# Kernel optimization log

Measured on AMD Instinct MI355X. Metric: run time of the kernel, lower is better.

## Reference

```python
import jax, jax.numpy as jnp
import numpy as np

B = 16
N = [4096, 1024, 256, 64, 16]
NF = [1, 16, 32, 64, 128, 256]
DEG = 6
KS = 5
LAT = 32


def spline_conv(x, edge_index, pseudo, W, root, bias):
    """SplineConv: open B-spline, degree 1, dim 3, kernel_size 5, sum aggregation (norm=False).
    x: [Nn, Cin], edge_index: [2, E] (src, dst), pseudo: [E, 3] in [0,1], W: [125, Cin, Cout]."""
    src, dst = edge_index[0], edge_index[1]
    v = pseudo * (KS - 1)                       # degree-1 open spline interval
    lo = jnp.clip(jnp.floor(v), 0.0, KS - 2)
    frac = v - lo                               # [E, 3]
    lo = lo.astype(jnp.int32)
    xs = x[src]                                 # [E, Cin] gather
    strides = jnp.array([1, KS, KS * KS], dtype=jnp.int32)
    msg = jnp.zeros((src.shape[0], W.shape[2]), dtype=x.dtype)
    for s in range(8):                          # (degree+1)^dim = 8 basis products
        bits = np.array([(s >> d) & 1 for d in range(3)], dtype=np.int32)
        basis = jnp.prod(jnp.where(bits[None, :] == 1, frac, 1.0 - frac), axis=1)  # [E]
        kidx = jnp.sum((lo + bits[None, :]) * strides[None, :], axis=1)            # [E]
        Wg = W[kidx]                                                               # [E, Cin, Cout]
        msg = msg + basis[:, None] * jnp.einsum('ei,eio->eo', xs, Wg)
    agg = jax.ops.segment_sum(msg, dst, num_segments=x.shape[0])
    return agg + x @ root + bias


def _fwd(fl, ei):
    (x, ea0, ea1, ea2, ea3, ea4, P01, P12, P23, P34, Pn1, P1n, P43, P32, P21, P10,
     W_c1, r_c1, b_c1, W_c2, r_c2, b_c2, W_c3, r_c3, b_c3, W_c4, r_c4, b_c4, W_c5, r_c5, b_c5,
     W_d5, r_d5, b_d5, W_d4, r_d4, b_d4, W_d3, r_d3, b_d3, W_d2, r_d2, b_d2, W_d1, r_d1, b_d1,
     fce1_w, fce1_b, fce21_w, fce21_b, fce22_w, fce22_b, fcd3_w, fcd3_b, fcd4_w, fcd4_b, eps) = fl
    ei0, ei1, ei2, ei3, ei4 = ei
    elu = jax.nn.elu
    # ---- encoder ----
    h = elu(spline_conv(x, ei0, ea0, W_c1, r_c1, b_c1))
    h = P01 @ h.reshape(B, N[0], NF[1])
    h = elu(spline_conv(h.reshape(-1, NF[1]), ei1, ea1, W_c2, r_c2, b_c2))
    h = P12 @ h.reshape(B, N[1], NF[2])
    h = elu(spline_conv(h.reshape(-1, NF[2]), ei2, ea2, W_c3, r_c3, b_c3))
    h = P23 @ h.reshape(B, N[2], NF[3])
    h = elu(spline_conv(h.reshape(-1, NF[3]), ei3, ea3, W_c4, r_c4, b_c4))
    h = P34 @ h.reshape(B, N[3], NF[4])
    h = elu(spline_conv(h.reshape(-1, NF[4]), ei4, ea4, W_c5, r_c5, b_c5))
    h = (Pn1 @ h.reshape(B, N[4], NF[5])).reshape(B, NF[5])
    # 1x1 convs over [B, C, 1, 1] == dense layers
    h = elu(h @ fce1_w + fce1_b)
    mu = h @ fce21_w + fce21_b
    logvar = h @ fce22_w + fce22_b
    # ---- reparameterize ----
    z = eps * jnp.exp(0.5 * logvar) + mu
    # ---- decoder ----
    h = elu(z @ fcd3_w + fcd3_b)
    h = elu(h @ fcd4_w + fcd4_b)
    h = P1n @ h.reshape(B, 1, NF[5])            # [B, N4, nf5]
    h = elu(spline_conv(h.reshape(-1, NF[5]), ei4, ea4, W_d5, r_d5, b_d5))
    h = P43 @ h.reshape(B, N[4], NF[4])
    h = elu(spline_conv(h.reshape(-1, NF[4]), ei3, ea3, W_d4, r_d4, b_d4))
    h = P32 @ h.reshape(B, N[3], NF[3])
    h = elu(spline_conv(h.reshape(-1, NF[3]), ei2, ea2, W_d3, r_d3, b_d3))
    h = P21 @ h.reshape(B, N[2], NF[2])
    h = elu(spline_conv(h.reshape(-1, NF[2]), ei1, ea1, W_d2, r_d2, b_d2))
    h = P10 @ h.reshape(B, N[1], NF[1])
    h = elu(spline_conv(h.reshape(-1, NF[1]), ei0, ea0, W_d1, r_d1, b_d1))
    recon = h.reshape(B, -1)                    # [B, N0] (nf0 == 1)
    return recon, mu, logvar


def setup_inputs() -> dict:
    key = jax.random.key(0)
    ks = iter(jax.random.split(key, 128))
    def nrm(shape, scale=1.0):
        return jax.random.normal(next(ks), shape, dtype=jnp.float32) * scale
    def edges(n):
        # per-sample random mesh-like connectivity, offset per graph copy
        e = jax.random.randint(next(ks), (2, B, n * DEG), 0, n)
        off = (jnp.arange(B) * n)[None, :, None]
        return (e + off).reshape(2, -1).astype(jnp.int32)
    inp = {}
    inp['x'] = nrm((B * N[0], NF[0]))
    for i in range(5):
        inp[f'ea{i}'] = jax.random.uniform(next(ks), (B * N[i] * DEG, 3), dtype=jnp.float32)
    pools = {'P01': (N[1], N[0]), 'P12': (N[2], N[1]), 'P23': (N[3], N[2]), 'P34': (N[4], N[3]),
             'Pn1': (1, N[4]), 'P1n': (N[4], 1), 'P43': (N[3], N[4]), 'P32': (N[2], N[3]),
             'P21': (N[1], N[2]), 'P10': (N[0], N[1])}
    for k2, (a, b) in pools.items():
        inp[k2] = nrm((a, b), 1.0 / np.sqrt(b))
    def spl(name, ci, co):
        inp[f'W_{name}'] = nrm((KS ** 3, ci, co), 0.1 / np.sqrt(ci))
        inp[f'r_{name}'] = nrm((ci, co), 1.0 / np.sqrt(ci))
        inp[f'b_{name}'] = nrm((co,), 0.01)
    spl('c1', NF[0], NF[1]); spl('c2', NF[1], NF[2]); spl('c3', NF[2], NF[3]); spl('c4', NF[3], NF[4]); spl('c5', NF[4], NF[5])
    spl('d5', NF[5], NF[4]); spl('d4', NF[4], NF[3]); spl('d3', NF[3], NF[2]); spl('d2', NF[2], NF[1]); spl('d1', NF[1], NF[0])
    def lin(name, ci, co):
        inp[f'{name}_w'] = nrm((ci, co), 1.0 / np.sqrt(ci))
        inp[f'{name}_b'] = nrm((co,), 0.01)
    lin('fce1', NF[5], NF[5]); lin('fce21', NF[5], LAT); lin('fce22', NF[5], LAT)
    lin('fcd3', LAT, NF[5]); lin('fcd4', NF[5], NF[5])
    inp['eps'] = nrm((B, LAT))
    for i in range(5):
        inp[f'ei{i}'] = edges(N[i])
    return inp


def reference(x, ea0, ea1, ea2, ea3, ea4, P01, P12, P23, P34, Pn1, P1n, P43, P32, P21, P10,
              W_c1, r_c1, b_c1, W_c2, r_c2, b_c2, W_c3, r_c3, b_c3, W_c4, r_c4, b_c4, W_c5, r_c5, b_c5,
              W_d5, r_d5, b_d5, W_d4, r_d4, b_d4, W_d3, r_d3, b_d3, W_d2, r_d2, b_d2, W_d1, r_d1, b_d1,
              fce1_w, fce1_b, fce21_w, fce21_b, fce22_w, fce22_b, fcd3_w, fcd3_b, fcd4_w, fcd4_b, eps,
              ei0, ei1, ei2, ei3, ei4):
    fl = (x, ea0, ea1, ea2, ea3, ea4, P01, P12, P23, P34, Pn1, P1n, P43, P32, P21, P10,
          W_c1, r_c1, b_c1, W_c2, r_c2, b_c2, W_c3, r_c3, b_c3, W_c4, r_c4, b_c4, W_c5, r_c5, b_c5,
          W_d5, r_d5, b_d5, W_d4, r_d4, b_d4, W_d3, r_d3, b_d3, W_d2, r_d2, b_d2, W_d1, r_d1, b_d1,
          fce1_w, fce1_b, fce21_w, fce21_b, fce22_w, fce22_b, fcd3_w, fcd3_b, fcd4_w, fcd4_b, eps)
    return _fwd(fl, (ei0, ei1, ei2, ei3, ei4))
```

## Files before the change

### kernel.cpp

```cpp
#include <hip/hip_runtime.h>
#include <hip/hip_bf16.h>

#define TPB 256
#define CDIV(a,b) (((a)+(b)-1)/(b))

__device__ __forceinline__ float elu_f(float v) {
    return v > 0.f ? v : expm1f(v);
}

__device__ __forceinline__ int ld_idx(const void* __restrict__ ei, int pos, int is64) {
    if (is64) return (int)((const long long*)ei)[pos];
    return ((const int*)ei)[pos];
}

__device__ __forceinline__ void spline_basis(const float* __restrict__ pseudo, int e,
                                             float bas[8], int kidx[8]) {
    float f[3]; int lo[3];
#pragma unroll
    for (int d = 0; d < 3; ++d) {
        float v = pseudo[e * 3 + d] * 4.f;
        float l = floorf(v);
        l = fminf(fmaxf(l, 0.f), 3.f);
        f[d] = v - l;
        lo[d] = (int)l;
    }
#pragma unroll
    for (int s = 0; s < 8; ++s) {
        int b0 = s & 1, b1 = (s >> 1) & 1, b2 = (s >> 2) & 1;
        bas[s] = (b0 ? f[0] : 1.f - f[0]) * (b1 ? f[1] : 1.f - f[1]) * (b2 ? f[2] : 1.f - f[2]);
        kidx[s] = (lo[0] + b0) + 5 * (lo[1] + b1) + 25 * (lo[2] + b2);
    }
}

__global__ void k_detect(const int* __restrict__ ei0_as_i32, int* __restrict__ flag) {
    if (threadIdx.x == 0 && blockIdx.x == 0) {
        int zeros = 0;
        for (int k = 0; k < 128; ++k)
            if (ei0_as_i32[2 * k + 1] == 0) zeros++;
        flag[0] = (zeros >= 120) ? 1 : 0;
    }
}

__global__ __launch_bounds__(TPB) void k_zero(float* __restrict__ p, int n) {
    int t = blockIdx.x * blockDim.x + threadIdx.x;
    if (t < n) p[t] = 0.f;
}

__global__ __launch_bounds__(TPB) void k_zero_i(int* __restrict__ p, int n) {
    int t = blockIdx.x * blockDim.x + threadIdx.x;
    if (t < n) p[t] = 0;
}

__global__ __launch_bounds__(TPB) void k_csr_count5(const void* e0, const void* e1,
                                                    const void* e2, const void* e3,
                                                    const void* e4, int* __restrict__ cnt,
                                                    const int* __restrict__ flag) {
    int t = blockIdx.x * blockDim.x + threadIdx.x;
    if (t >= 523776) return;
    int is64 = flag[0];
    const void* ei; int e, E, noff;
    if (t < 393216)      { ei = e0; e = t;          E = 393216; noff = 0; }
    else if (t < 491520) { ei = e1; e = t - 393216; E = 98304;  noff = 65536; }
    else if (t < 516096) { ei = e2; e = t - 491520; E = 24576;  noff = 81920; }
    else if (t < 522240) { ei = e3; e = t - 516096; E = 6144;   noff = 86016; }
    else                 { ei = e4; e = t - 522240; E = 1536;   noff = 87040; }
    int dst = ld_idx(ei, E + e, is64);
    atomicAdd(&cnt[noff + dst], 1);
}

__device__ __forceinline__ void lvl_of_block(int b, int& l, int& lb) {
    if (b < 256)      { l = 0; lb = b; }
    else if (b < 320) { l = 1; lb = b - 256; }
    else if (b < 336) { l = 2; lb = b - 320; }
    else if (b < 340) { l = 3; lb = b - 336; }
    else              { l = 4; lb = b - 340; }
}

__global__ __launch_bounds__(256) void k_scan_a(const int* __restrict__ cnt,
                                                int* __restrict__ rows,
                                                int* __restrict__ bsum) {
    const int NOFF[5] = {0, 65536, 81920, 86016, 87040};
    const int ROFF[5] = {0, 65537, 81922, 86019, 87044};
    __shared__ int s[256];
    int l, lb; lvl_of_block(blockIdx.x, l, lb);
    int t = threadIdx.x;
    int i = lb * 256 + t;
    int v = cnt[NOFF[l] + i];
    s[t] = v;
    __syncthreads();
    for (int off = 1; off < 256; off <<= 1) {
        int u = (t >= off) ? s[t - off] : 0;
        __syncthreads();
        s[t] += u;
        __syncthreads();
    }
    rows[ROFF[l] + i] = s[t] - v;
    if (t == 255) bsum[blockIdx.x] = s[255];
}

__global__ __launch_bounds__(256) void k_scan_b(int* __restrict__ bsum,
                                                int* __restrict__ rows) {
    const int NB[5]    = {256, 64, 16, 4, 1};
    const int BOFF[5]  = {0, 256, 320, 336, 340};
    const int ROFF[5]  = {0, 65537, 81922, 86019, 87044};
    const int NODES[5] = {65536, 16384, 4096, 1024, 256};
    __shared__ int s[256];
    int l = blockIdx.x, t = threadIdx.x;
    int nb = NB[l];
    int v = (t < nb) ? bsum[BOFF[l] + t] : 0;
    s[t] = v;
    __syncthreads();
    for (int off = 1; off < 256; off <<= 1) {
        int u = (t >= off) ? s[t - off] : 0;
        __syncthreads();
        s[t] += u;
        __syncthreads();
    }
    if (t < nb) bsum[BOFF[l] + t] = s[t] - v;
    if (t == 0) rows[ROFF[l] + NODES[l]] = s[255];
}

__global__ __launch_bounds__(256) void k_scan_c(const int* __restrict__ bsum,
                                                int* __restrict__ rows) {
    const int ROFF[5] = {0, 65537, 81922, 86019, 87044};
    int l, lb; lvl_of_block(blockIdx.x, l, lb);
    rows[ROFF[l] + lb * 256 + threadIdx.x] += bsum[blockIdx.x];
}

__global__ __launch_bounds__(TPB) void k_csr_fill5(const void* e0, const void* e1,
                                                   const void* e2, const void* e3,
                                                   const void* e4,
                                                   const int* __restrict__ rows,
                                                   int* __restrict__ cur,
                                                   int* __restrict__ eids,
                                                   const int* __restrict__ flag) {
    int t = blockIdx.x * blockDim.x + threadIdx.x;
    if (t >= 523776) return;
    int is64 = flag[0];
    const void* ei; int e, E, noff, roff, eoff;
    if (t < 393216)      { ei = e0; e = t;          E = 393216; noff = 0;     roff = 0;     eoff = 0; }
    else if (t < 491520) { ei = e1; e = t - 393216; E = 98304;  noff = 65536; roff = 65537; eoff = 393216; }
    else if (t < 516096) { ei = e2; e = t - 491520; E = 24576;  noff = 81920; roff = 81922; eoff = 491520; }
    else if (t < 522240) { ei = e3; e = t - 516096; E = 6144;   noff = 86016; roff = 86019; eoff = 516096; }
    else                 { ei = e4; e = t - 522240; E = 1536;   noff = 87040; roff = 87044; eoff = 522240; }
    int dst = ld_idx(ei, E + e, is64);
    int pos = rows[roff + dst] + atomicAdd(&cur[noff + dst], 1);
    eids[eoff + pos] = e;
}

__global__ __launch_bounds__(TPB) void k_csr_count(const void* __restrict__ ei,
                                                   int* __restrict__ cnt, int E,
                                                   const int* __restrict__ flag) {
    int t = blockIdx.x * blockDim.x + threadIdx.x;
    if (t >= E) return;
    int dst = ld_idx(ei, E + t, flag[0]);
    atomicAdd(&cnt[dst], 1);
}

__global__ __launch_bounds__(1024) void k_csr_scan(const int* __restrict__ cnt,
                                                   int* __restrict__ row_ptr) {
    __shared__ int s_part[1024];
    int t = threadIdx.x;
    int base = t * 64;
    int sum = 0;
    for (int i = 0; i < 64; ++i) sum += cnt[base + i];
    s_part[t] = sum;
    __syncthreads();
    for (int off = 1; off < 1024; off <<= 1) {
        int v = (t >= off) ? s_part[t - off] : 0;
        __syncthreads();
        s_part[t] += v;
        __syncthreads();
    }
    int run = (t == 0) ? 0 : s_part[t - 1];
    for (int i = 0; i < 64; ++i) { row_ptr[base + i] = run; run += cnt[base + i]; }
    if (t == 1023) row_ptr[65536] = run;
}

__global__ __launch_bounds__(TPB) void k_csr_fill(const void* __restrict__ ei,
                                                  const int* __restrict__ row_ptr,
                                                  int* __restrict__ cur,
                                                  int* __restrict__ eid, int E,
                                                  const int* __restrict__ flag) {
    int t = blockIdx.x * blockDim.x + threadIdx.x;
    if (t >= E) return;
    int dst = ld_idx(ei, E + t, flag[0]);
    int pos = row_ptr[dst] + atomicAdd(&cur[dst], 1);
    eid[pos] = t;
}

__global__ __launch_bounds__(256) void k_gather_c1(const float* __restrict__ x,
                                                   const float* __restrict__ pseudo,
                                                   const void* __restrict__ ei,
                                                   const float* __restrict__ W,
                                                   const float* __restrict__ root,
                                                   const float* __restrict__ bias,
                                                   const int* __restrict__ row_ptr,
                                                   const int* __restrict__ eid,
                                                   float* __restrict__ agg,
                                                   const int* __restrict__ flag) {
    __shared__ float4 s_w[500];
    for (int i = threadIdx.x; i < 500; i += 256)
        s_w[i] = reinterpret_cast<const float4*>(W)[i];
    __syncthreads();
    int t = blockIdx.x * 256 + threadIdx.x;
    int n = t >> 2, cg = t & 3, co0 = cg * 4;
    int is64 = flag[0];
    float xn = x[n];
    float a0 = fmaf(xn, root[co0 + 0], bias[co0 + 0]);
    float a1 = fmaf(xn, root[co0 + 1], bias[co0 + 1]);
    float a2 = fmaf(xn, root[co0 + 2], bias[co0 + 2]);
    float a3 = fmaf(xn, root[co0 + 3], bias[co0 + 3]);
    int rb = row_ptr[n], re = row_ptr[n + 1];
    for (int idx = rb; idx < re; ++idx) {
        int e = eid[idx];
        int src = ld_idx(ei, e, is64);
        float bas[8]; int kidx[8];
        spline_basis(pseudo, e, bas, kidx);
        float xs = x[src];
        float m0 = 0.f, m1 = 0.f, m2 = 0.f, m3 = 0.f;
#pragma unroll
        for (int s = 0; s < 8; ++s) {
            float4 w = s_w[kidx[s] * 4 + cg];
            float bs = bas[s];
            m0 = fmaf(bs, w.x, m0);
            m1 = fmaf(bs, w.y, m1);
            m2 = fmaf(bs, w.z, m2);
            m3 = fmaf(bs, w.w, m3);
        }
        a0 = fmaf(xs, m0, a0);
        a1 = fmaf(xs, m1, a1);
        a2 = fmaf(xs, m2, a2);
        a3 = fmaf(xs, m3, a3);
    }
    float4 v = make_float4(a0, a1, a2, a3);
    *reinterpret_cast<float4*>(&agg[n * 16 + co0]) = v;
}

__global__ __launch_bounds__(256) void k_gather_d1(const float* __restrict__ xin,
                                                   const float* __restrict__ pseudo,
                                                   const void* __restrict__ ei,
                                                   const float* __restrict__ W,
                                                   const float* __restrict__ root,
                                                   const float* __restrict__ bias,
                                                   const int* __restrict__ row_ptr,
                                                   const int* __restrict__ eid,
                                                   float* __restrict__ outp,
                                                   const int* __restrict__ flag) {
    __shared__ float s_w[2000];
    for (int i = threadIdx.x; i < 2000; i += 256) s_w[i] = W[i];
    __syncthreads();
    int t = blockIdx.x * 256 + threadIdx.x;
    int n = t >> 2, l = t & 3;
    int is64 = flag[0];
    int rb = row_ptr[n], re = row_ptr[n + 1];
    float acc = 0.f;
    for (int idx = rb + l; idx < re; idx += 4) {
        int e = eid[idx];
        int src = ld_idx(ei, e, is64);
        float bas[8]; int kidx[8];
        spline_basis(pseudo, e, bas, kidx);
        const float4* xs4 = reinterpret_cast<const float4*>(xin + src * 16);
        float4 xv0 = xs4[0], xv1 = xs4[1], xv2 = xs4[2], xv3 = xs4[3];
        float m = 0.f;
#pragma unroll
        for (int s = 0; s < 8; ++s) {
            const float4* wp = reinterpret_cast<const float4*>(s_w + kidx[s] * 16);
            float4 w0 = wp[0], w1 = wp[1], w2 = wp[2], w3 = wp[3];
            float p = 0.f;
            p = fmaf(xv0.x, w0.x, p); p = fmaf(xv0.y, w0.y, p);
            p = fmaf(xv0.z, w0.z, p); p = fmaf(xv0.w, w0.w, p);
            p = fmaf(xv1.x, w1.x, p); p = fmaf(xv1.y, w1.y, p);
            p = fmaf(xv1.z, w1.z, p); p = fmaf(xv1.w, w1.w, p);
            p = fmaf(xv2.x, w2.x, p); p = fmaf(xv2.y, w2.y, p);
            p = fmaf(xv2.z, w2.z, p); p = fmaf(xv2.w, w2.w, p);
            p = fmaf(xv3.x, w3.x, p); p = fmaf(xv3.y, w3.y, p);
            p = fmaf(xv3.z, w3.z, p); p = fmaf(xv3.w, w3.w, p);
            m = fmaf(bas[s], p, m);
        }
        acc += m;
    }
    acc += __shfl_xor(acc, 1);
    acc += __shfl_xor(acc, 2);
    if (l == 0) {
        const float4* xr = reinterpret_cast<const float4*>(xin + n * 16);
        const float4* rr = reinterpret_cast<const float4*>(root);
        float r = bias[0];
#pragma unroll
        for (int q = 0; q < 4; ++q) {
            float4 xv = xr[q], rv = rr[q];
            r = fmaf(xv.x, rv.x, r); r = fmaf(xv.y, rv.y, r);
            r = fmaf(xv.z, rv.z, r); r = fmaf(xv.w, rv.w, r);
        }
        outp[n] = elu_f(r + acc);
    }
}

template <int CIN, int COUT, int CSPLIT, int IROOT>
__global__ __launch_bounds__(256) void k_gW2(const float* __restrict__ x,
                                             const float* __restrict__ pseudo,
                                             const void* __restrict__ ei,
                                             const float* __restrict__ W,
                                             const float* __restrict__ root,
                                             const float* __restrict__ bias,
                                             const int* __restrict__ row_ptr,
                                             const int* __restrict__ eid,
                                             float* __restrict__ agg,
                                             const int* __restrict__ flag) {
    constexpr int COG = COUT / 4;
    constexpr int CPT = CIN / CSPLIT;
    constexpr int PS = CPT + 1;
    __shared__ float4 s_w[125 * PS];
    int cg = blockIdx.y, cih = blockIdx.z;
    const float4* W4 = reinterpret_cast<const float4*>(W);
    for (int i = threadIdx.x; i < 125 * CPT; i += 256) {
        int k = i / CPT, ci = i - k * CPT;
        s_w[k * PS + ci] = W4[(k * CIN + cih * CPT + ci) * COG + cg];
    }
    __syncthreads();
    int nl = threadIdx.x >> 2, l = threadIdx.x & 3;
    int n = blockIdx.x * 64 + nl;
    int is64 = flag[0];
    int co0 = cg * 4;
    float4 acc = make_float4(0.f, 0.f, 0.f, 0.f);
    if (IROOT == 1 || (IROOT == 2 && cih == 0)) {
        if (l == 0) acc = reinterpret_cast<const float4*>(bias)[cg];
        constexpr int CQ = CIN / 4;
        const float* xp = x + (size_t)n * CIN + l * CQ;
        const float4* r4 = reinterpret_cast<const float4*>(root) + (size_t)(l * CQ) * COG + cg;
#pragma unroll 4
        for (int ci = 0; ci < CQ; ++ci) {
            float xv = xp[ci];
            float4 rv = r4[ci * COG];
            acc.x = fmaf(xv, rv.x, acc.x); acc.y = fmaf(xv, rv.y, acc.y);
            acc.z = fmaf(xv, rv.z, acc.z); acc.w = fmaf(xv, rv.w, acc.w);
        }
    }
    int rb = row_ptr[n], re = row_ptr[n + 1];
    for (int idx = rb + l; idx < re; idx += 4) {
        int e = eid[idx];
        int src = ld_idx(ei, e, is64);
        float bas[8]; int kidx[8];
        spline_basis(pseudo, e, bas, kidx);
        float xv[CPT];
        const float* xp = x + (size_t)src * CIN + cih * CPT;
#pragma unroll
        for (int ci = 0; ci < CPT; ++ci) xv[ci] = xp[ci];
#pragma unroll
        for (int s = 0; s < 8; ++s) {
            const float4* wp = s_w + kidx[s] * PS;
            float bs = bas[s];
#pragma unroll
            for (int ci = 0; ci < CPT; ++ci) {
                float bx = bs * xv[ci];
                float4 w = wp[ci];
                acc.x = fmaf(bx, w.x, acc.x); acc.y = fmaf(bx, w.y, acc.y);
                acc.z = fmaf(bx, w.z, acc.z); acc.w = fmaf(bx, w.w, acc.w);
            }
        }
    }
    acc.x += __shfl_xor(acc.x, 1); acc.y += __shfl_xor(acc.y, 1);
    acc.z += __shfl_xor(acc.z, 1); acc.w += __shfl_xor(acc.w, 1);
    acc.x += __shfl_xor(acc.x, 2); acc.y += __shfl_xor(acc.y, 2);
    acc.z += __shfl_xor(acc.z, 2); acc.w += __shfl_xor(acc.w, 2);
    if (l == 0) {
        float* o = agg + (size_t)n * COUT + co0;
        if (IROOT == 1) {
            *reinterpret_cast<float4*>(o) = acc;
        } else {
            atomicAdd(o + 0, acc.x); atomicAdd(o + 1, acc.y);
            atomicAdd(o + 2, acc.z); atomicAdd(o + 3, acc.w);
        }
    }
}

__global__ __launch_bounds__(TPB) void k_root4(const float* __restrict__ x,
                                               const float* __restrict__ root,
                                               const float* __restrict__ bias,
                                               float* __restrict__ out,
                                               int nnode, int cin, int cout) {
    int t = blockIdx.x * blockDim.x + threadIdx.x;
    if (t >= nnode * cout) return;
    int n = t / cout, co = t - n * cout;
    const float4* xr = reinterpret_cast<const float4*>(x + n * cin);
    float a0 = 0.f, a1 = 0.f, a2 = 0.f, a3 = 0.f;
    int q4 = cin >> 2;
    for (int q = 0; q < q4; ++q) {
        float4 xv = xr[q];
        const float* rp = root + (q * 4) * cout + co;
        a0 = fmaf(xv.x, rp[0], a0);
        a1 = fmaf(xv.y, rp[cout], a1);
        a2 = fmaf(xv.z, rp[2 * cout], a2);
        a3 = fmaf(xv.w, rp[3 * cout], a3);
    }
    out[t] = bias[co] + ((a0 + a1) + (a2 + a3));
}

template <int CIN, int COUT, int CSPLIT>
__global__ __launch_bounds__(TPB) void k_msg4(const float* __restrict__ x,
                                              const float* __restrict__ pseudo,
                                              const void* __restrict__ ei,
                                              const float* __restrict__ W,
                                              float* __restrict__ agg, int E,
                                              const int* __restrict__ flag) {
    constexpr int COG = COUT / 4;
    constexpr int CPT = CIN / CSPLIT;
    int t = blockIdx.x * blockDim.x + threadIdx.x;
    if (t >= E * COG * CSPLIT) return;
    int is64 = flag[0];
    int cog = t % COG;
    int rest = t / COG;
    int cs = rest % CSPLIT;
    int e = rest / CSPLIT;
    int co0 = cog * 4;
    int src = ld_idx(ei, e, is64);
    int dst = ld_idx(ei, E + e, is64);
    float bas[8]; int kidx[8];
    spline_basis(pseudo, e, bas, kidx);
    int wof[8];
#pragma unroll
    for (int s = 0; s < 8; ++s) wof[s] = kidx[s] * CIN * COUT + co0;
    float a0 = 0.f, a1 = 0.f, a2 = 0.f, a3 = 0.f;
    const float* xp = x + src * CIN + cs * CPT;
    const int cbase = cs * CPT * COUT;
    for (int ci = 0; ci < CPT; ++ci) {
        float xv = xp[ci];
        int off = cbase + ci * COUT;
#pragma unroll
        for (int s = 0; s < 8; ++s) {
            float4 w = *reinterpret_cast<const float4*>(&W[wof[s] + off]);
            float bx = bas[s] * xv;
            a0 = fmaf(bx, w.x, a0);
            a1 = fmaf(bx, w.y, a1);
            a2 = fmaf(bx, w.z, a2);
            a3 = fmaf(bx, w.w, a3);
        }
    }
    float* ap = &agg[dst * COUT + co0];
    atomicAdd(ap + 0, a0);
    atomicAdd(ap + 1, a1);
    atomicAdd(ap + 2, a2);
    atomicAdd(ap + 3, a3);
}

template <int CIN, int COUT>
__global__ __launch_bounds__(TPB) void k_msg_s(const float* __restrict__ x,
                                               const float* __restrict__ pseudo,
                                               const void* __restrict__ ei,
                                               const float* __restrict__ W,
                                               float* __restrict__ agg, int E,
                                               const int* __restrict__ flag) {
    int t = blockIdx.x * blockDim.x + threadIdx.x;
    if (t >= E * COUT) return;
    int is64 = flag[0];
    int e = t / COUT, co = t - e * COUT;
    int src = ld_idx(ei, e, is64);
    int dst = ld_idx(ei, E + e, is64);
    float bas[8]; int kidx[8];
    spline_basis(pseudo, e, bas, kidx);
    float acc = 0.f;
    const float* xp = x + src * CIN;
    for (int ci = 0; ci < CIN; ++ci) {
        float xv = xp[ci];
#pragma unroll
        for (int s = 0; s < 8; ++s)
            acc = fmaf(bas[s] * xv, W[kidx[s] * CIN * COUT + ci * COUT + co], acc);
    }
    atomicAdd(&agg[dst * COUT + co], acc);
}

__global__ __launch_bounds__(1024) void k_msg_c1(const float* __restrict__ x,
                                                 const float* __restrict__ pseudo,
                                                 const void* __restrict__ ei,
                                                 const float* __restrict__ W,
                                                 const float* __restrict__ root,
                                                 const float* __restrict__ bias,
                                                 float* __restrict__ agg,
                                                 const int* __restrict__ flag) {
    __shared__ float s_acc[4096 * 4];
    __shared__ float s_w[125 * 4];
    int b = blockIdx.x, cg = blockIdx.y, t = threadIdx.x;
    int co0 = cg * 4;
    int is64 = flag[0];
    if (t < 500) s_w[t] = W[(t >> 2) * 16 + co0 + (t & 3)];
    float r0 = root[co0], r1 = root[co0 + 1], r2 = root[co0 + 2], r3 = root[co0 + 3];
    float b0 = bias[co0], b1 = bias[co0 + 1], b2 = bias[co0 + 2], b3 = bias[co0 + 3];
    for (int n = t; n < 4096; n += 1024) {
        float xv = x[b * 4096 + n];
        s_acc[n * 4 + 0] = fmaf(xv, r0, b0);
        s_acc[n * 4 + 1] = fmaf(xv, r1, b1);
        s_acc[n * 4 + 2] = fmaf(xv, r2, b2);
        s_acc[n * 4 + 3] = fmaf(xv, r3, b3);
    }
    __syncthreads();
    int ebeg = b * 24576;
    for (int k = t; k < 24576; k += 1024) {
        int e = ebeg + k;
        int src = ld_idx(ei, e, is64);
        int dst = ld_idx(ei, 393216 + e, is64);
        float xv = x[src];
        float bas[8]; int kidx[8];
        spline_basis(pseudo, e, bas, kidx);
        float m0 = 0.f, m1 = 0.f, m2 = 0.f, m3 = 0.f;
#pragma unroll
        for (int s = 0; s < 8; ++s) {
            const float* wp = s_w + kidx[s] * 4;
            float bs = bas[s];
            m0 = fmaf(bs, wp[0], m0);
            m1 = fmaf(bs, wp[1], m1);
            m2 = fmaf(bs, wp[2], m2);
            m3 = fmaf(bs, wp[3], m3);
        }
        int dl = (dst - b * 4096) * 4;
        atomicAdd(&s_acc[dl + 0], m0 * xv);
        atomicAdd(&s_acc[dl + 1], m1 * xv);
        atomicAdd(&s_acc[dl + 2], m2 * xv);
        atomicAdd(&s_acc[dl + 3], m3 * xv);
    }
    __syncthreads();
    for (int n = t; n < 4096; n += 1024) {
        float4 v = *reinterpret_cast<float4*>(&s_acc[n * 4]);
        *reinterpret_cast<float4*>(&agg[(b * 4096 + n) * 16 + co0]) = v;
    }
}

template <int F, int ELU>
__global__ __launch_bounds__(256) void k_pool2(const float* __restrict__ in,
                                               const float* __restrict__ P,
                                               float* __restrict__ out,
                                               int nout, int nin) {
    constexpr int FQ = F / 4;
    constexpr int TI = 256 / FQ;
    constexpr int KT = 64;
    constexpr int PS = KT + 4;
    __shared__ float s_p[TI * PS];
    __shared__ float4 s_in[KT * FQ];
    int tid = threadIdx.x;
    int fq = tid % FQ;
    int i = tid / FQ;
    int b = blockIdx.y;
    int gi = blockIdx.x * TI + i;
    int nchunk = nin / gridDim.z;
    int kbeg = blockIdx.z * nchunk;
    const float4* inb4 = reinterpret_cast<const float4*>(in + b * nin * F);
    float4 acc = make_float4(0.f, 0.f, 0.f, 0.f);

    for (int k0 = kbeg; k0 < kbeg + nchunk; k0 += KT) {
        __syncthreads();
        for (int idx = tid; idx < TI * (KT / 4); idx += 256) {
            int r = idx / (KT / 4), c = idx % (KT / 4);
            float4 v = *reinterpret_cast<const float4*>(&P[(blockIdx.x * TI + r) * nin + k0 + c * 4]);
            *reinterpret_cast<float4*>(&s_p[r * PS + c * 4]) = v;
        }
        for (int idx = tid; idx < KT * FQ; idx += 256) {
            float4 v = inb4[(size_t)(k0 + idx / FQ) * FQ + (idx % FQ)];
            if (ELU) {
                v.x = elu_f(v.x); v.y = elu_f(v.y);
                v.z = elu_f(v.z); v.w = elu_f(v.w);
            }
            s_in[idx] = v;
        }
        __syncthreads();
#pragma unroll 4
        for (int j = 0; j < KT; j += 4) {
            float4 pv = *reinterpret_cast<const float4*>(&s_p[i * PS + j]);
            float4 v0 = s_in[(j + 0) * FQ + fq];
            float4 v1 = s_in[(j + 1) * FQ + fq];
            float4 v2 = s_in[(j + 2) * FQ + fq];
            float4 v3 = s_in[(j + 3) * FQ + fq];
            acc.x = fmaf(pv.x, v0.x, acc.x); acc.y = fmaf(pv.x, v0.y, acc.y);
            acc.z = fmaf(pv.x, v0.z, acc.z); acc.w = fmaf(pv.x, v0.w, acc.w);
            acc.x = fmaf(pv.y, v1.x, acc.x); acc.y = fmaf(pv.y, v1.y, acc.y);
            acc.z = fmaf(pv.y, v1.z, acc.z); acc.w = fmaf(pv.y, v1.w, acc.w);
            acc.x = fmaf(pv.z, v2.x, acc.x); acc.y = fmaf(pv.z, v2.y, acc.y);
            acc.z = fmaf(pv.z, v2.z, acc.z); acc.w = fmaf(pv.z, v2.w, acc.w);
            acc.x = fmaf(pv.w, v3.x, acc.x); acc.y = fmaf(pv.w, v3.y, acc.y);
            acc.z = fmaf(pv.w, v3.z, acc.z); acc.w = fmaf(pv.w, v3.w, acc.w);
        }
    }
    float* o = out + ((size_t)b * nout + gi) * F + fq * 4;
    if (gridDim.z > 1) {
        atomicAdd(o + 0, acc.x); atomicAdd(o + 1, acc.y);
        atomicAdd(o + 2, acc.z); atomicAdd(o + 3, acc.w);
    } else {
        *reinterpret_cast<float4*>(o) = acc;
    }
}

__global__ __launch_bounds__(TPB) void k_pool_e(const float* __restrict__ in,
                                                const float* __restrict__ P,
                                                float* __restrict__ out,
                                                int nout, int nin, int F, int elu) {
    int t = blockIdx.x * blockDim.x + threadIdx.x;
    if (t >= 16 * nout * F) return;
    int f = t % F;
    int rest = t / F;
    int i = rest % nout;
    int b = rest / nout;
    const float* ip = in + b * nin * F + f;
    const float* pp = P + i * nin;
    float acc = 0.f;
    if (elu) {
#pragma unroll 4
        for (int j = 0; j < nin; ++j) acc = fmaf(pp[j], elu_f(ip[j * F]), acc);
    } else {
#pragma unroll 4
        for (int j = 0; j < nin; ++j) acc = fmaf(pp[j], ip[j * F], acc);
    }
    out[t] = acc;
}

__global__ __launch_bounds__(1024) void k_fc_fused2(
        const float* __restrict__ c5agg, const float* __restrict__ Pn1,
        const float* __restrict__ fce1_w, const float* __restrict__ fce1_b,
        const float* __restrict__ fce21_w, const float* __restrict__ fce21_b,
        const float* __restrict__ fce22_w, const float* __restrict__ fce22_b,
        const float* __restrict__ eps,
        const float* __restrict__ fcd3_w, const float* __restrict__ fcd3_b,
        const float* __restrict__ fcd4_w, const float* __restrict__ fcd4_b,
        const float* __restrict__ P1n,
        float* __restrict__ out_mu, float* __restrict__ out_lv,
        float* __restrict__ dec_in) {
    __shared__ float s0[256], s1[256], sz[32], sp[1024];
    int b = blockIdx.x, t = threadIdx.x;
    if (t < 256) {
        const float* ap = c5agg + b * 4096 + t;
        float acc = 0.f;
#pragma unroll
        for (int n = 0; n < 16; ++n) acc = fmaf(Pn1[n], elu_f(ap[n * 256]), acc);
        s0[t] = acc;
    }
    __syncthreads();
    {
        int q = t >> 8, co = t & 255;
        const float* w = fce1_w + co;
        float a = 0.f;
        int c0 = q * 64;
        for (int ci = 0; ci < 64; ci += 8) {
#pragma unroll
            for (int k = 0; k < 8; ++k) a = fmaf(s0[c0 + ci + k], w[(c0 + ci + k) * 256], a);
        }
        sp[t] = a;
    }
    __syncthreads();
    if (t < 256) s1[t] = elu_f(sp[t] + sp[t + 256] + sp[t + 512] + sp[t + 768] + fce1_b[t]);
    __syncthreads();
    if (t < 512) {
        int which = t >> 8, r = t & 255;
        int co = r & 31, q = r >> 5;
        const float* w = (which ? fce22_w : fce21_w) + co;
        float a = 0.f;
        int c0 = q * 32;
#pragma unroll
        for (int k = 0; k < 32; ++k) a = fmaf(s1[c0 + k], w[(c0 + k) * 32], a);
        sp[t] = a;
    }
    __syncthreads();
    if (t < 64) {
        int which = t >> 5, co = t & 31;
        float m = (which ? fce22_b : fce21_b)[co];
        int base = which * 256 + co;
#pragma unroll
        for (int q = 0; q < 8; ++q) m += sp[base + q * 32];
        if (which == 0) { out_mu[b * 32 + co] = m; s0[co] = m; }
        else            { out_lv[b * 32 + co] = m; s0[64 + co] = m; }
    }
    __syncthreads();
    if (t < 32) sz[t] = fmaf(eps[b * 32 + t], expf(0.5f * s0[64 + t]), s0[t]);
    __syncthreads();
    if (t < 256) {
        float d = fcd3_b[t];
#pragma unroll
        for (int ci = 0; ci < 32; ++ci) d = fmaf(sz[ci], fcd3_w[ci * 256 + t], d);
        s0[t] = elu_f(d);
    }
    __syncthreads();
    {
        int q = t >> 8, co = t & 255;
        const float* w = fcd4_w + co;
        float a = 0.f;
        int c0 = q * 64;
        for (int ci = 0; ci < 64; ci += 8) {
#pragma unroll
            for (int k = 0; k < 8; ++k) a = fmaf(s0[c0 + ci + k], w[(c0 + ci + k) * 256], a);
        }
        sp[t] = a;
    }
    __syncthreads();
    if (t < 256) s1[t] = elu_f(sp[t] + sp[t + 256] + sp[t + 512] + sp[t + 768] + fcd4_b[t]);
    __syncthreads();
    {
        float* op = dec_in + b * 4096;
        for (int idx = t; idx < 4096; idx += 1024) {
            int n = idx >> 8, f = idx & 255;
            op[idx] = P1n[n] * s1[f];
        }
    }
}

__global__ __launch_bounds__(TPB) void k_elu_out(const float* __restrict__ in,
                                                 float* __restrict__ out, int n) {
    int t = blockIdx.x * blockDim.x + threadIdx.x;
    if (t < n) out[t] = elu_f(in[t]);
}

extern "C" void kernel_launch(void* const* d_in, const int* in_sizes, int n_in,
                              void* d_out, int out_size, void* d_ws, size_t ws_size,
                              hipStream_t stream) {
    const float* x    = (const float*)d_in[0];
    const float* ea0  = (const float*)d_in[1];
    const float* ea1  = (const float*)d_in[2];
    const float* ea2  = (const float*)d_in[3];
    const float* ea3  = (const float*)d_in[4];
    const float* ea4  = (const float*)d_in[5];
    const float* P01  = (const float*)d_in[6];
    const float* P12  = (const float*)d_in[7];
    const float* P23  = (const float*)d_in[8];
    const float* P34  = (const float*)d_in[9];
    const float* Pn1  = (const float*)d_in[10];
    const float* P1n  = (const float*)d_in[11];
    const float* P43  = (const float*)d_in[12];
    const float* P32  = (const float*)d_in[13];
    const float* P21  = (const float*)d_in[14];
    const float* P10  = (const float*)d_in[15];
    const float* W_c1 = (const float*)d_in[16]; const float* r_c1 = (const float*)d_in[17]; const float* b_c1 = (const float*)d_in[18];
    const float* W_c2 = (const float*)d_in[19]; const float* r_c2 = (const float*)d_in[20]; const float* b_c2 = (const float*)d_in[21];
    const float* W_c3 = (const float*)d_in[22]; const float* r_c3 = (const float*)d_in[23]; const float* b_c3 = (const float*)d_in[24];
    const float* W_c4 = (const float*)d_in[25]; const float* r_c4 = (const float*)d_in[26]; const float* b_c4 = (const float*)d_in[27];
    const float* W_c5 = (const float*)d_in[28]; const float* r_c5 = (const float*)d_in[29]; const float* b_c5 = (const float*)d_in[30];
    const float* W_d5 = (const float*)d_in[31]; const float* r_d5 = (const float*)d_in[32]; const float* b_d5 = (const float*)d_in[33];
    const float* W_d4 = (const float*)d_in[34]; const float* r_d4 = (const float*)d_in[35]; const float* b_d4 = (const float*)d_in[36];
    const float* W_d3 = (const float*)d_in[37]; const float* r_d3 = (const float*)d_in[38]; const float* b_d3 = (const float*)d_in[39];
    const float* W_d2 = (const float*)d_in[40]; const float* r_d2 = (const float*)d_in[41]; const float* b_d2 = (const float*)d_in[42];
    const float* W_d1 = (const float*)d_in[43]; const float* r_d1 = (const float*)d_in[44]; const float* b_d1 = (const float*)d_in[45];
    const float* fce1_w  = (const float*)d_in[46]; const float* fce1_b  = (const float*)d_in[47];
    const float* fce21_w = (const float*)d_in[48]; const float* fce21_b = (const float*)d_in[49];
    const float* fce22_w = (const float*)d_in[50]; const float* fce22_b = (const float*)d_in[51];
    const float* fcd3_w  = (const float*)d_in[52]; const float* fcd3_b  = (const float*)d_in[53];
    const float* fcd4_w  = (const float*)d_in[54]; const float* fcd4_b  = (const float*)d_in[55];
    const float* eps  = (const float*)d_in[56];
    const void* ei0 = d_in[57];
    const void* ei1 = d_in[58];
    const void* ei2 = d_in[59];
    const void* ei3 = d_in[60];
    const void* ei4 = d_in[61];

    const int E0 = 393216, E1 = 98304, E2 = 24576, E3 = 6144, E4 = 1536;
    const int N0 = 65536, N1 = 16384, N2 = 4096, N3 = 1024, N4 = 256;

    float* sm   = (float*)d_ws;
    float* bufA = sm + 13824;
    float* bufB = bufA + 1048576;
    int*  flag  = (int*)(bufB + 262144);
    int*  ibase = flag + 64;
    int* cur  = ibase;
    int* rows = cur + 87296;
    int* eids = rows + 87301;
    int* bsum = eids + 523776;
    const size_t WS_ALL = (size_t)(13824 + 1048576 + 262144 + 64 + 87296 + 87301 + 523776 + 512) * 4;
    int* o_row = ibase;
    int* o_cur = o_row + 65537;
    int* o_eid = o_cur + 65536;
    const size_t WS_OLD = (size_t)(13824 + 1048576 + 262144 + 64 + 524352) * 4;
    const bool bigA = ws_size >= WS_ALL;
    const bool big0 = ws_size >= WS_OLD;

    const int ROFF[5] = {0, 65537, 81922, 86019, 87044};
    const int EOFF[5] = {0, 393216, 491520, 516096, 522240};

    float* out = (float*)d_out;
    float* out_mu = out + 65536;
    float* out_lv = out + 66048;

    auto g = [](int n) { return dim3((unsigned)CDIV(n, TPB)); };

    k_detect<<<1, 64, 0, stream>>>((const int*)ei0, flag);

    if (bigA) {
        k_zero_i<<<g(87296), TPB, 0, stream>>>(cur, 87296);
        k_csr_count5<<<g(523776), TPB, 0, stream>>>(ei0, ei1, ei2, ei3, ei4, cur, flag);
        k_scan_a<<<341, 256, 0, stream>>>(cur, rows, bsum);
        k_scan_b<<<5, 256, 0, stream>>>(bsum, rows);
        k_scan_c<<<341, 256, 0, stream>>>(bsum, rows);
        k_zero_i<<<g(87296), TPB, 0, stream>>>(cur, 87296);
        k_csr_fill5<<<g(523776), TPB, 0, stream>>>(ei0, ei1, ei2, ei3, ei4, rows, cur, eids, flag);

        k_gather_c1<<<1024, 256, 0, stream>>>(x, ea0, ei0, W_c1, r_c1, b_c1,
                                              rows + ROFF[0], eids + EOFF[0], bufA, flag);
        k_zero<<<g(262144), TPB, 0, stream>>>(bufB, 262144);
        k_pool2<16, 1><<<dim3(16, 16, 8), 256, 0, stream>>>(bufA, P01, bufB, 1024, 4096);

        k_zero<<<g(524288), TPB, 0, stream>>>(bufA, 524288);
        k_gW2<16, 32, 2, 2><<<dim3(256, 8, 2), 256, 0, stream>>>(bufB, ea1, ei1, W_c2, r_c2, b_c2,
                                                                 rows + ROFF[1], eids + EOFF[1], bufA, flag);
        k_zero<<<g(131072), TPB, 0, stream>>>(bufB, 131072);
        k_pool2<32, 1><<<dim3(8, 16, 4), 256, 0, stream>>>(bufA, P12, bufB, 256, 1024);

        k_zero<<<g(262144), TPB, 0, stream>>>(bufA, 262144);
        k_gW2<32, 64, 4, 2><<<dim3(64, 16, 4), 256, 0, stream>>>(bufB, ea2, ei2, W_c3, r_c3, b_c3,
                                                                 rows + ROFF[2], eids + EOFF[2], bufA, flag);
        k_zero<<<g(65536), TPB, 0, stream>>>(bufB, 65536);
        k_pool2<64, 1><<<dim3(4, 16, 2), 256, 0, stream>>>(bufA, P23, bufB, 64, 256);

        k_zero<<<g(131072), TPB, 0, stream>>>(bufA, 131072);
        k_gW2<64, 128, 8, 2><<<dim3(16, 32, 8), 256, 0, stream>>>(bufB, ea3, ei3, W_c4, r_c4, b_c4,
                                                                  rows + ROFF[3], eids + EOFF[3], bufA, flag);
        k_pool_e<<<g(16 * 16 * 128), TPB, 0, stream>>>(bufA, P34, bufB, 16, 64, 128, 1);

        k_zero<<<g(65536), TPB, 0, stream>>>(bufA, 65536);
        k_gW2<128, 256, 16, 2><<<dim3(4, 64, 16), 256, 0, stream>>>(bufB, ea4, ei4, W_c5, r_c5, b_c5,
                                                                    rows + ROFF[4], eids + EOFF[4], bufA, flag);

        k_fc_fused2<<<16, 1024, 0, stream>>>(bufA, Pn1,
                                             fce1_w, fce1_b, fce21_w, fce21_b, fce22_w, fce22_b,
                                             eps, fcd3_w, fcd3_b, fcd4_w, fcd4_b, P1n,
                                             out_mu, out_lv, bufA);

        k_zero<<<g(32768), TPB, 0, stream>>>(bufB, 32768);
        k_gW2<256, 128, 32, 2><<<dim3(4, 32, 32), 256, 0, stream>>>(bufA, ea4, ei4, W_d5, r_d5, b_d5,
                                                                    rows + ROFF[4], eids + EOFF[4], bufB, flag);
        k_pool_e<<<g(16 * 64 * 128), TPB, 0, stream>>>(bufB, P43, bufA, 64, 16, 128, 1);

        k_zero<<<g(65536), TPB, 0, stream>>>(bufB, 65536);
        k_gW2<128, 64, 16, 2><<<dim3(16, 16, 16), 256, 0, stream>>>(bufA, ea3, ei3, W_d4, r_d4, b_d4,
                                                                    rows + ROFF[3], eids + EOFF[3], bufB, flag);
        k_pool2<64, 1><<<dim3(16, 16, 1), 256, 0, stream>>>(bufB, P32, bufA, 256, 64);

        k_zero<<<g(131072), TPB, 0, stream>>>(bufB, 131072);
        k_gW2<64, 32, 8, 2><<<dim3(64, 8, 8), 256, 0, stream>>>(bufA, ea2, ei2, W_d3, r_d3, b_d3,
                                                                rows + ROFF[2], eids + EOFF[2], bufB, flag);
        k_zero<<<g(524288), TPB, 0, stream>>>(bufA, 524288);
        k_pool2<32, 1><<<dim3(32, 16, 2), 256, 0, stream>>>(bufB, P21, bufA, 1024, 256);

        k_zero<<<g(262144), TPB, 0, stream>>>(bufB, 262144);
        k_gW2<32, 16, 4, 2><<<dim3(256, 4, 4), 256, 0, stream>>>(bufA, ea1, ei1, W_d2, r_d2, b_d2,
                                                                 rows + ROFF[1], eids + EOFF[1], bufB, flag);
        k_zero<<<g(1048576), TPB, 0, stream>>>(bufA, 1048576);
        k_pool2<16, 1><<<dim3(64, 16, 2), 256, 0, stream>>>(bufB, P10, bufA, 4096, 1024);

        k_gather_d1<<<1024, 256, 0, stream>>>(bufA, ea0, ei0, W_d1, r_d1, b_d1,
                                              rows + ROFF[0], eids + EOFF[0], out, flag);
        return;
    }

    if (big0) {
        k_zero_i<<<g(65536), TPB, 0, stream>>>(o_cur, 65536);
        k_csr_count<<<g(E0), TPB, 0, stream>>>(ei0, o_cur, E0, flag);
        k_csr_scan<<<1, 1024, 0, stream>>>(o_cur, o_row);
        k_zero_i<<<g(65536), TPB, 0, stream>>>(o_cur, 65536);
        k_csr_fill<<<g(E0), TPB, 0, stream>>>(ei0, o_row, o_cur, o_eid, E0, flag);
        k_gather_c1<<<1024, 256, 0, stream>>>(x, ea0, ei0, W_c1, r_c1, b_c1,
                                              o_row, o_eid, bufA, flag);
    } else {
        k_msg_c1<<<dim3(16, 4), 1024, 0, stream>>>(x, ea0, ei0, W_c1, r_c1, b_c1, bufA, flag);
    }
    k_zero<<<g(262144), TPB, 0, stream>>>(bufB, 262144);
    k_pool2<16, 1><<<dim3(16, 16, 4), 256, 0, stream>>>(bufA, P01, bufB, 1024, 4096);

    k_root4<<<g(N1 * 32), TPB, 0, stream>>>(bufB, r_c2, b_c2, bufA, N1, 16, 32);
    k_msg4<16, 32, 1><<<g(E1 * 8), TPB, 0, stream>>>(bufB, ea1, ei1, W_c2, bufA, E1, flag);
    k_zero<<<g(131072), TPB, 0, stream>>>(bufB, 131072);
    k_pool2<32, 1><<<dim3(8, 16, 2), 256, 0, stream>>>(bufA, P12, bufB, 256, 1024);

    k_root4<<<g(N2 * 64), TPB, 0, stream>>>(bufB, r_c3, b_c3, bufA, N2, 32, 64);
    k_msg4<32, 64, 1><<<g(E2 * 16), TPB, 0, stream>>>(bufB, ea2, ei2, W_c3, bufA, E2, flag);
    k_zero<<<g(65536), TPB, 0, stream>>>(bufB, 65536);
    k_pool2<64, 1><<<dim3(4, 16, 2), 256, 0, stream>>>(bufA, P23, bufB, 64, 256);

    k_root4<<<g(N3 * 128), TPB, 0, stream>>>(bufB, r_c4, b_c4, bufA, N3, 64, 128);
    k_msg4<64, 128, 1><<<g(E3 * 32), TPB, 0, stream>>>(bufB, ea3, ei3, W_c4, bufA, E3, flag);
    k_pool_e<<<g(16 * 16 * 128), TPB, 0, stream>>>(bufA, P34, bufB, 16, 64, 128, 1);

    k_root4<<<g(N4 * 256), TPB, 0, stream>>>(bufB, r_c5, b_c5, bufA, N4, 128, 256);
    k_msg4<128, 256, 2><<<g(E4 * 128), TPB, 0, stream>>>(bufB, ea4, ei4, W_c5, bufA, E4, flag);

    k_fc_fused2<<<16, 1024, 0, stream>>>(bufA, Pn1,
                                         fce1_w, fce1_b, fce21_w, fce21_b, fce22_w, fce22_b,
                                         eps, fcd3_w, fcd3_b, fcd4_w, fcd4_b, P1n,
                                         out_mu, out_lv, bufA);

    k_root4<<<g(N4 * 128), TPB, 0, stream>>>(bufA, r_d5, b_d5, bufB, N4, 256, 128);
    k_msg4<256, 128, 4><<<g(E4 * 128), TPB, 0, stream>>>(bufA, ea4, ei4, W_d5, bufB, E4, flag);
    k_pool_e<<<g(16 * 64 * 128), TPB, 0, stream>>>(bufB, P43, bufA, 64, 16, 128, 1);

    k_root4<<<g(N3 * 64), TPB, 0, stream>>>(bufA, r_d4, b_d4, bufB, N3, 128, 64);
    k_msg4<128, 64, 2><<<g(E3 * 32), TPB, 0, stream>>>(bufA, ea3, ei3, W_d4, bufB, E3, flag);
    k_pool2<64, 1><<<dim3(16, 16, 1), 256, 0, stream>>>(bufB, P32, bufA, 256, 64);

    k_root4<<<g(N2 * 32), TPB, 0, stream>>>(bufA, r_d3, b_d3, bufB, N2, 64, 32);
    k_msg4<64, 32, 1><<<g(E2 * 8), TPB, 0, stream>>>(bufA, ea2, ei2, W_d3, bufB, E2, flag);
    k_pool2<32, 1><<<dim3(32, 16, 1), 256, 0, stream>>>(bufB, P21, bufA, 1024, 256);

    k_root4<<<g(N1 * 16), TPB, 0, stream>>>(bufA, r_d2, b_d2, bufB, N1, 32, 16);
    k_msg4<32, 16, 1><<<g(E1 * 4), TPB, 0, stream>>>(bufA, ea1, ei1, W_d2, bufB, E1, flag);
    k_pool2<16, 1><<<dim3(64, 16, 1), 256, 0, stream>>>(bufB, P10, bufA, 4096, 1024);

    if (big0) {
        k_gather_d1<<<1024, 256, 0, stream>>>(bufA, ea0, ei0, W_d1, r_d1, b_d1,
                                              o_row, o_eid, out, flag);
    } else {
        k_root4<<<g(N0 * 1), TPB, 0, stream>>>(bufA, r_d1, b_d1, bufB, N0, 16, 1);
        k_msg_s<16, 1><<<g(E0), TPB, 0, stream>>>(bufA, ea0, ei0, W_d1, bufB, E0, flag);
        k_elu_out<<<g(N0), TPB, 0, stream>>>(bufB, out, 65536);
    }
}
```

Measured before the change: 980.2 us.

## Loop over input-channel slices in-kernel instead of splitting across blocks with atomics

The gather spline-conv kernel no longer splits input channels across grid z-blocks that combine results with atomicAdd into zeroed buffers. Each block now loops over 8-channel weight slices, reloading shared memory per slice, and writes its result directly with one float4 store. This removes the atomics and the zeroing kernels before each conv. Deeper layers also use 16 lanes per node instead of 4. The cost is fewer blocks (less parallelism), extra barriers per slice, and longer per-block serial work.

```diff
diff --git a/kernel.cpp b/kernel.cpp
--- a/kernel.cpp
+++ b/kernel.cpp
@@ -296,8 +296,8 @@
     }
 }
 
-template <int CIN, int COUT, int CSPLIT, int IROOT>
-__global__ __launch_bounds__(256) void k_gW2(const float* __restrict__ x,
+template <int CIN, int COUT, int LANES>
+__global__ __launch_bounds__(256) void k_gW3(const float* __restrict__ x,
                                              const float* __restrict__ pseudo,
                                              const void* __restrict__ ei,
                                              const float* __restrict__ W,
@@ -308,24 +308,22 @@
                                              float* __restrict__ agg,
                                              const int* __restrict__ flag) {
     constexpr int COG = COUT / 4;
-    constexpr int CPT = CIN / CSPLIT;
+    constexpr int CPT = 8;
+    constexpr int CSLICES = CIN / CPT;
     constexpr int PS = CPT + 1;
+    constexpr int NL = 256 / LANES;
     __shared__ float4 s_w[125 * PS];
-    int cg = blockIdx.y, cih = blockIdx.z;
+    int cg = blockIdx.y;
+    int co0 = cg * 4;
+    int nl = threadIdx.x / LANES, l = threadIdx.x % LANES;
+    int n = blockIdx.x * NL + nl;
+    int is64 = flag[0];
     const float4* W4 = reinterpret_cast<const float4*>(W);
-    for (int i = threadIdx.x; i < 125 * CPT; i += 256) {
-        int k = i / CPT, ci = i - k * CPT;
-        s_w[k * PS + ci] = W4[(k * CIN + cih * CPT + ci) * COG + cg];
-    }
-    __syncthreads();
-    int nl = threadIdx.x >> 2, l = threadIdx.x & 3;
-    int n = blockIdx.x * 64 + nl;
-    int is64 = flag[0];
-    int co0 = cg * 4;
+
     float4 acc = make_float4(0.f, 0.f, 0.f, 0.f);
-    if (IROOT == 1 || (IROOT == 2 && cih == 0)) {
+    {
         if (l == 0) acc = reinterpret_cast<const float4*>(bias)[cg];
-        constexpr int CQ = CIN / 4;
+        constexpr int CQ = CIN / LANES;
         const float* xp = x + (size_t)n * CIN + l * CQ;
         const float4* r4 = reinterpret_cast<const float4*>(root) + (size_t)(l * CQ) * COG + cg;
 #pragma unroll 4
@@ -337,40 +335,45 @@
         }
     }
     int rb = row_ptr[n], re = row_ptr[n + 1];
-    for (int idx = rb + l; idx < re; idx += 4) {
-        int e = eid[idx];
-        int src = ld_idx(ei, e, is64);
-        float bas[8]; int kidx[8];
-        spline_basis(pseudo, e, bas, kidx);
-        float xv[CPT];
-        const float* xp = x + (size_t)src * CIN + cih * CPT;
-#pragma unroll
-        for (int ci = 0; ci < CPT; ++ci) xv[ci] = xp[ci];
-#pragma unroll
-        for (int s = 0; s < 8; ++s) {
-            const float4* wp = s_w + kidx[s] * PS;
-            float bs = bas[s];
-#pragma unroll
-            for (int ci = 0; ci < CPT; ++ci) {
-                float bx = bs * xv[ci];
-                float4 w = wp[ci];
-                acc.x = fmaf(bx, w.x, acc.x); acc.y = fmaf(bx, w.y, acc.y);
-                acc.z = fmaf(bx, w.z, acc.z); acc.w = fmaf(bx, w.w, acc.w);
+
+    for (int cih = 0; cih < CSLICES; ++cih) {
+        __syncthreads();
+        for (int i = threadIdx.x; i < 125 * CPT; i += 256) {
+            int k = i / CPT, ci = i - k * CPT;
+            s_w[k * PS + ci] = W4[(k * CIN + cih * CPT + ci) * COG + cg];
+        }
+        __syncthreads();
+        for (int idx = rb + l; idx < re; idx += LANES) {
+            int e = eid[idx];
+            int src = ld_idx(ei, e, is64);
+            float bas[8]; int kidx[8];
+            spline_basis(pseudo, e, bas, kidx);
+            float xv[CPT];
+            const float* xp = x + (size_t)src * CIN + cih * CPT;
+#pragma unroll
+            for (int ci = 0; ci < CPT; ++ci) xv[ci] = xp[ci];
+#pragma unroll
+            for (int s = 0; s < 8; ++s) {
+                const float4* wp = s_w + kidx[s] * PS;
+                float bs = bas[s];
+#pragma unroll
+                for (int ci = 0; ci < CPT; ++ci) {
+                    float bx = bs * xv[ci];
+                    float4 w = wp[ci];
+                    acc.x = fmaf(bx, w.x, acc.x); acc.y = fmaf(bx, w.y, acc.y);
+                    acc.z = fmaf(bx, w.z, acc.z); acc.w = fmaf(bx, w.w, acc.w);
+                }
             }
         }
     }
-    acc.x += __shfl_xor(acc.x, 1); acc.y += __shfl_xor(acc.y, 1);
-    acc.z += __shfl_xor(acc.z, 1); acc.w += __shfl_xor(acc.w, 1);
-    acc.x += __shfl_xor(acc.x, 2); acc.y += __shfl_xor(acc.y, 2);
-    acc.z += __shfl_xor(acc.z, 2); acc.w += __shfl_xor(acc.w, 2);
+#pragma unroll
+    for (int off = 1; off < LANES; off <<= 1) {
+        acc.x += __shfl_xor(acc.x, off); acc.y += __shfl_xor(acc.y, off);
+        acc.z += __shfl_xor(acc.z, off); acc.w += __shfl_xor(acc.w, off);
+    }
     if (l == 0) {
         float* o = agg + (size_t)n * COUT + co0;
-        if (IROOT == 1) {
-            *reinterpret_cast<float4*>(o) = acc;
-        } else {
-            atomicAdd(o + 0, acc.x); atomicAdd(o + 1, acc.y);
-            atomicAdd(o + 2, acc.z); atomicAdd(o + 3, acc.w);
-        }
+        *reinterpret_cast<float4*>(o) = acc;
     }
 }
 
@@ -790,51 +793,43 @@
         k_zero<<<g(262144), TPB, 0, stream>>>(bufB, 262144);
         k_pool2<16, 1><<<dim3(16, 16, 8), 256, 0, stream>>>(bufA, P01, bufB, 1024, 4096);
 
-        k_zero<<<g(524288), TPB, 0, stream>>>(bufA, 524288);
-        k_gW2<16, 32, 2, 2><<<dim3(256, 8, 2), 256, 0, stream>>>(bufB, ea1, ei1, W_c2, r_c2, b_c2,
-                                                                 rows + ROFF[1], eids + EOFF[1], bufA, flag);
+        k_gW3<16, 32, 4><<<dim3(256, 8), 256, 0, stream>>>(bufB, ea1, ei1, W_c2, r_c2, b_c2,
+                                                           rows + ROFF[1], eids + EOFF[1], bufA, flag);
         k_zero<<<g(131072), TPB, 0, stream>>>(bufB, 131072);
         k_pool2<32, 1><<<dim3(8, 16, 4), 256, 0, stream>>>(bufA, P12, bufB, 256, 1024);
 
-        k_zero<<<g(262144), TPB, 0, stream>>>(bufA, 262144);
-        k_gW2<32, 64, 4, 2><<<dim3(64, 16, 4), 256, 0, stream>>>(bufB, ea2, ei2, W_c3, r_c3, b_c3,
-                                                                 rows + ROFF[2], eids + EOFF[2], bufA, flag);
+        k_gW3<32, 64, 4><<<dim3(64, 16), 256, 0, stream>>>(bufB, ea2, ei2, W_c3, r_c3, b_c3,
+                                                           rows + ROFF[2], eids + EOFF[2], bufA, flag);
         k_zero<<<g(65536), TPB, 0, stream>>>(bufB, 65536);
         k_pool2<64, 1><<<dim3(4, 16, 2), 256, 0, stream>>>(bufA, P23, bufB, 64, 256);
 
-        k_zero<<<g(131072), TPB, 0, stream>>>(bufA, 131072);
-        k_gW2<64, 128, 8, 2><<<dim3(16, 32, 8), 256, 0, stream>>>(bufB, ea3, ei3, W_c4, r_c4, b_c4,
-                                                                  rows + ROFF[3], eids + EOFF[3], bufA, flag);
+        k_gW3<64, 128, 16><<<dim3(64, 32), 256, 0, stream>>>(bufB, ea3, ei3, W_c4, r_c4, b_c4,
+                                                             rows + ROFF[3], eids + EOFF[3], bufA, flag);
         k_pool_e<<<g(16 * 16 * 128), TPB, 0, stream>>>(bufA, P34, bufB, 16, 64, 128, 1);
 
-        k_zero<<<g(65536), TPB, 0, stream>>>(bufA, 65536);
-        k_gW2<128, 256, 16, 2><<<dim3(4, 64, 16), 256, 0, stream>>>(bufB, ea4, ei4, W_c5, r_c5, b_c5,
-                                                                    rows + ROFF[4], eids + EOFF[4], bufA, flag);
+        k_gW3<128, 256, 16><<<dim3(16, 64), 256, 0, stream>>>(bufB, ea4, ei4, W_c5, r_c5, b_c5,
+                                                              rows + ROFF[4], eids + EOFF[4], bufA, flag);
 
         k_fc_fused2<<<16, 1024, 0, stream>>>(bufA, Pn1,
                                              fce1_w, fce1_b, fce21_w, fce21_b, fce22_w, fce22_b,
                                              eps, fcd3_w, fcd3_b, fcd4_w, fcd4_b, P1n,
                                              out_mu, out_lv, bufA);
 
-        k_zero<<<g(32768), TPB, 0, stream>>>(bufB, 32768);
-        k_gW2<256, 128, 32, 2><<<dim3(4, 32, 32), 256, 0, stream>>>(bufA, ea4, ei4, W_d5, r_d5, b_d5,
-                                                                    rows + ROFF[4], eids + EOFF[4], bufB, flag);
+        k_gW3<256, 128, 16><<<dim3(16, 32), 256, 0, stream>>>(bufA, ea4, ei4, W_d5, r_d5, b_d5,
+                                                              rows + ROFF[4], eids + EOFF[4], bufB, flag);
         k_pool_e<<<g(16 * 64 * 128), TPB, 0, stream>>>(bufB, P43, bufA, 64, 16, 128, 1);
 
-        k_zero<<<g(65536), TPB, 0, stream>>>(bufB, 65536);
-        k_gW2<128, 64, 16, 2><<<dim3(16, 16, 16), 256, 0, stream>>>(bufA, ea3, ei3, W_d4, r_d4, b_d4,
-                                                                    rows + ROFF[3], eids + EOFF[3], bufB, flag);
+        k_gW3<128, 64, 16><<<dim3(64, 16), 256, 0, stream>>>(bufA, ea3, ei3, W_d4, r_d4, b_d4,
+                                                             rows + ROFF[3], eids + EOFF[3], bufB, flag);
         k_pool2<64, 1><<<dim3(16, 16, 1), 256, 0, stream>>>(bufB, P32, bufA, 256, 64);
 
-        k_zero<<<g(131072), TPB, 0, stream>>>(bufB, 131072);
-        k_gW2<64, 32, 8, 2><<<dim3(64, 8, 8), 256, 0, stream>>>(bufA, ea2, ei2, W_d3, r_d3, b_d3,
-                                                                rows + ROFF[2], eids + EOFF[2], bufB, flag);
+        k_gW3<64, 32, 4><<<dim3(64, 8), 256, 0, stream>>>(bufA, ea2, ei2, W_d3, r_d3, b_d3,
+                                                          rows + ROFF[2], eids + EOFF[2], bufB, flag);
         k_zero<<<g(524288), TPB, 0, stream>>>(bufA, 524288);
         k_pool2<32, 1><<<dim3(32, 16, 2), 256, 0, stream>>>(bufB, P21, bufA, 1024, 256);
 
-        k_zero<<<g(262144), TPB, 0, stream>>>(bufB, 262144);
-        k_gW2<32, 16, 4, 2><<<dim3(256, 4, 4), 256, 0, stream>>>(bufA, ea1, ei1, W_d2, r_d2, b_d2,
-                                                                 rows + ROFF[1], eids + EOFF[1], bufB, flag);
+        k_gW3<32, 16, 4><<<dim3(256, 4), 256, 0, stream>>>(bufA, ea1, ei1, W_d2, r_d2, b_d2,
+                                                           rows + ROFF[1], eids + EOFF[1], bufB, flag);
         k_zero<<<g(1048576), TPB, 0, stream>>>(bufA, 1048576);
         k_pool2<16, 1><<<dim3(64, 16, 2), 256, 0, stream>>>(bufB, P10, bufA, 4096, 1024);
 
```

Measured after the change: 1.014 ms. +3.4%, slower.
